# Kernel optimization log

Measured on AMD Instinct MI355X. Metric: run time of the kernel, lower is better.

Reference implementation:

```python
import jax, jax.numpy as jnp
import numpy as np

B, T, I, H = 64, 1024, 256, 512


def setup_inputs() -> dict:
    key = jax.random.key(0)
    ks = jax.random.split(key, 5)
    # Xavier-uniform-like scale: sqrt(6/(fan_in+fan_out)) ~ use small normal init
    def xavier(k, shape):
        bound = np.sqrt(6.0 / (shape[0] + shape[1])).astype(np.float32)
        return jax.random.uniform(k, shape, jnp.float32, -bound, bound)
    return {
        "x": jax.random.normal(ks[0], (B, T, I), jnp.float32),
        "W_ih0": xavier(ks[1], (I, H)),
        "W_hh0": xavier(ks[2], (H, H)),
        "b0": jnp.zeros((H,), jnp.float32),
        "W_ih1": xavier(ks[3], (H, H)),
        "W_hh1": xavier(ks[4], (H, H)),
        "b1": jnp.zeros((H,), jnp.float32),
    }


def _run_layer(xs, W_ih, W_hh, b):
    # xs: [B, T, D_in] -> ys: [B, T, H], h_last: [B, H]
    h0 = jnp.zeros((xs.shape[0], W_hh.shape[0]), xs.dtype)
    # Precompute input transform for all timesteps in one big GEMM
    x_proj = jnp.einsum('btd,dh->bth', xs, W_ih)

    def step(h, xp_t):
        h_new = jnp.tanh(xp_t + h @ W_hh + b)
        return h_new, h_new

    h_last, ys = jax.lax.scan(step, h0, jnp.swapaxes(x_proj, 0, 1))  # scan over T
    return jnp.swapaxes(ys, 0, 1), h_last


def reference(x, W_ih0, W_hh0, b0, W_ih1, W_hh1, b1):
    out0, h0n = _run_layer(x, W_ih0, W_hh0, b0)
    out1, h1n = _run_layer(out0, W_ih1, W_hh1, b1)
    h_n = jnp.stack([h0n, h1n], axis=0)  # [num_layers, B, H]
    return out1, h_n
```

## Files before the change

kernel.cpp:

```cpp
#include <hip/hip_runtime.h>
#include <cstdint>

#define B_  64
#define T_  1024
#define I_  256
#define H_  512

typedef _Float16 h2_t __attribute__((ext_vector_type(2)));
typedef int sv16 __attribute__((ext_vector_type(16)));

__device__ __forceinline__ uint16_t f2h(float f) {
  _Float16 h = (_Float16)f;
  return __builtin_bit_cast(uint16_t, h);
}
__device__ __forceinline__ float dot2(uint32_t a, uint32_t b, float c) {
  return __builtin_amdgcn_fdot2(__builtin_bit_cast(h2_t, a),
                                __builtin_bit_cast(h2_t, b), c, false);
}
__device__ __forceinline__ float fast_tanh(float s) {
  float e = __expf(2.0f * s);
  return fmaf(-2.0f, __builtin_amdgcn_rcpf(e + 1.0f), 1.0f);
}

template<int P>
__device__ __forceinline__ uint32_t hsel(sv16 h0, sv16 h1, sv16 h2, sv16 h3) {
  if constexpr (P < 16)      return (uint32_t)h0[P];
  else if constexpr (P < 32) return (uint32_t)h1[P - 16];
  else if constexpr (P < 48) return (uint32_t)h2[P - 32];
  else                       return (uint32_t)h3[P - 48];
}

__global__ void pack_whh(const float* __restrict__ W, uint32_t* __restrict__ out) {
  int idx = blockIdx.x * 256 + threadIdx.x;
  int k8 = idx >> 11;
  int j  = (idx >> 2) & 511;
  int m  = idx & 3;
  int k  = k8 * 8 + m * 2;
  uint32_t lo = f2h(W[k * H_ + j]);
  uint32_t hi = f2h(W[(k + 1) * H_ + j]);
  out[idx] = lo | (hi << 16);
}

template<int K>
__global__ __launch_bounds__(256) void gemm_rows(const float* A,
    const float* __restrict__ W, const float* __restrict__ bias,
    float* Y) {
  __shared__ float As[64 * (K + 1)];
  const int tid = threadIdx.x;
  const size_t row0 = (size_t)blockIdx.x * 64;
  const float* Ab = A + row0 * K;
  for (int idx = tid * 4; idx < 64 * K; idx += 1024) {
    float4 v = *(const float4*)(Ab + idx);
    int rr = idx / K;
    int cc = idx - rr * K;
    float* dst = &As[rr * (K + 1) + cc];
    dst[0] = v.x; dst[1] = v.y; dst[2] = v.z; dst[3] = v.w;
  }
  __syncthreads();
  const int cg = tid & 15;
  const int rg = tid >> 4;
  float acc[4][32];
  #pragma unroll
  for (int i = 0; i < 32; ++i) {
    float bz = bias[cg + 16 * i];
    acc[0][i] = bz; acc[1][i] = bz; acc[2][i] = bz; acc[3][i] = bz;
  }
  const float* Wc = W + cg;
  for (int k = 0; k < K; ++k) {
    float a0 = As[(rg * 4 + 0) * (K + 1) + k];
    float a1 = As[(rg * 4 + 1) * (K + 1) + k];
    float a2 = As[(rg * 4 + 2) * (K + 1) + k];
    float a3 = As[(rg * 4 + 3) * (K + 1) + k];
    const float* Wk = Wc + (size_t)k * H_;
    #pragma unroll
    for (int i = 0; i < 32; ++i) {
      float w = Wk[16 * i];
      acc[0][i] = fmaf(a0, w, acc[0][i]);
      acc[1][i] = fmaf(a1, w, acc[1][i]);
      acc[2][i] = fmaf(a2, w, acc[2][i]);
      acc[3][i] = fmaf(a3, w, acc[3][i]);
    }
  }
  float* Yb = Y + row0 * H_;
  #pragma unroll
  for (int jj = 0; jj < 4; ++jj) {
    float* Yr = Yb + (size_t)(rg * 4 + jj) * H_ + cg;
    #pragma unroll
    for (int i = 0; i < 32; ++i) Yr[16 * i] = acc[jj][i];
  }
}

#define ROW(m, WEXPR) { uint4 w_ = (WEXPR); \
  a0 = dot2(w_.x, hsel<4*(m)+0>(h0,h1,h2,h3), a0); \
  a1 = dot2(w_.y, hsel<4*(m)+1>(h0,h1,h2,h3), a1); \
  a2 = dot2(w_.z, hsel<4*(m)+2>(h0,h1,h2,h3), a2); \
  a3 = dot2(w_.w, hsel<4*(m)+3>(h0,h1,h2,h3), a3); }

#define BATCH_LOAD(OFF0, OFF1, OFF2, OFF3) \
  asm volatile("s_load_dwordx16 %0, %4, " OFF0 "\n\t" \
               "s_load_dwordx16 %1, %4, " OFF1 "\n\t" \
               "s_load_dwordx16 %2, %4, " OFF2 "\n\t" \
               "s_load_dwordx16 %3, %4, " OFF3 \
               : "=s"(h0), "=s"(h1), "=s"(h2), "=s"(h3) : "s"(hbase)); \
  asm volatile("s_waitcnt lgkmcnt(0)" : "+s"(h0), "+s"(h1), "+s"(h2), "+s"(h3)); \
  __builtin_amdgcn_sched_barrier(0);

#define CONS16(W0)  ROW(0,W0(0))  ROW(1,W0(1))  ROW(2,W0(2))  ROW(3,W0(3)) \
                    ROW(4,W0(4))  ROW(5,W0(5))  ROW(6,W0(6))  ROW(7,W0(7)) \
                    ROW(8,W0(8))  ROW(9,W0(9))  ROW(10,W0(10)) ROW(11,W0(11)) \
                    ROW(12,W0(12)) ROW(13,W0(13)) ROW(14,W0(14)) ROW(15,W0(15))

#define WREG0(m) wrv[m]
#define WREG1(m) wrv[16 + (m)]
#define WLDS(m)  WL[(m) * 512 + j]
#define WSTR(m)  g[m]

__global__ __launch_bounds__(512, 2) void rnn_scan(float* Y,
    const uint4* __restrict__ Wp, ushort* __restrict__ hb16,
    float* __restrict__ hn) {
  __shared__ uint4 WL[16 * 512];
  const int j = threadIdx.x;
  float* Yb = Y + (size_t)blockIdx.x * (T_ * H_);
  ushort* hbp = hb16 + blockIdx.x * H_;

  uint4 wrv[32];
  #pragma unroll
  for (int m = 0; m < 32; ++m) wrv[m] = Wp[m * H_ + j];
  #pragma unroll
  for (int it = 0; it < 16; ++it) WL[it * 512 + j] = Wp[(32 + it) * 512 + j];

  float xp0 = Yb[j];
  float v = fast_tanh(xp0);
  hbp[j] = f2h(v);
  Yb[j] = v;
  const uint64_t hbase = (uint64_t)(uintptr_t)hbp;
  asm volatile("s_waitcnt vmcnt(0) lgkmcnt(0)\n\ts_barrier\n\ts_dcache_inv" ::: "memory");

  for (int t = 1; t < T_; ++t) {
    float xpt = Yb[t * H_ + j];
    uint4 g[16];
    #pragma unroll
    for (int m = 0; m < 16; ++m) g[m] = Wp[(48 + m) * H_ + j];
    float a0 = 0.f, a1 = 0.f, a2 = 0.f, a3 = 0.f;
    sv16 h0, h1, h2, h3;
    BATCH_LOAD("0x0", "0x40", "0x80", "0xc0")
    CONS16(WREG0)
    BATCH_LOAD("0x100", "0x140", "0x180", "0x1c0")
    CONS16(WREG1)
    BATCH_LOAD("0x200", "0x240", "0x280", "0x2c0")
    CONS16(WLDS)
    BATCH_LOAD("0x300", "0x340", "0x380", "0x3c0")
    CONS16(WSTR)

    float s = xpt + ((a0 + a1) + (a2 + a3));
    v = fast_tanh(s);
    hbp[j] = f2h(v);
    Yb[t * H_ + j] = v;
    asm volatile("s_waitcnt vmcnt(0)\n\ts_barrier\n\ts_dcache_inv" ::: "memory");
  }
  hn[blockIdx.x * H_ + j] = v;
}

extern "C" void kernel_launch(void* const* d_in, const int* in_sizes, int n_in,
                              void* d_out, int out_size, void* d_ws, size_t ws_size,
                              hipStream_t stream) {
  const float* x     = (const float*)d_in[0];
  const float* W_ih0 = (const float*)d_in[1];
  const float* W_hh0 = (const float*)d_in[2];
  const float* b0    = (const float*)d_in[3];
  const float* W_ih1 = (const float*)d_in[4];
  const float* W_hh1 = (const float*)d_in[5];
  const float* b1    = (const float*)d_in[6];

  float* Y  = (float*)d_out;
  float* hn = Y + (size_t)B_ * T_ * H_;
  uint32_t* Wp = (uint32_t*)d_ws;
  ushort* hbuf = (ushort*)((char*)d_ws + 512 * 1024);

  pack_whh<<<512, 256, 0, stream>>>(W_hh0, Wp);
  gemm_rows<I_><<<1024, 256, 0, stream>>>(x, W_ih0, b0, Y);
  rnn_scan<<<B_, H_, 0, stream>>>(Y, (const uint4*)Wp, hbuf, hn);
  pack_whh<<<512, 256, 0, stream>>>(W_hh1, Wp);
  gemm_rows<H_><<<1024, 256, 0, stream>>>(Y, W_ih1, b1, Y);
  rnn_scan<<<B_, H_, 0, stream>>>(Y, (const uint4*)Wp, hbuf, hn + B_ * H_);
}
```

Measured before the change: 4.183 ms.

## Keep more W_hh in registers, drop LDS, double-buffer hidden state

The recurrent kernel now keeps 48 of the 64 packed W_hh row groups in VGPRs and drops the LDS copy. The remaining 16 groups are streamed from global memory in four-chunk pieces, each prefetched one batch ahead so the load overlaps the dot-product work. The fp16 hidden state is ping-ponged between two buffers, and the barrier is moved ahead of the Y store so that store is no longer waited on before the next step. The cost is much higher register pressure (192 VGPRs for weights under launch_bounds 512,2), which risks spills, and the hidden-state workspace doubles in size.

```diff
diff --git a/kernel.cpp b/kernel.cpp
--- a/kernel.cpp
+++ b/kernel.cpp
@@ -100,63 +100,79 @@
   asm volatile("s_load_dwordx16 %0, %4, " OFF0 "\n\t" \
                "s_load_dwordx16 %1, %4, " OFF1 "\n\t" \
                "s_load_dwordx16 %2, %4, " OFF2 "\n\t" \
-               "s_load_dwordx16 %3, %4, " OFF3 \
-               : "=s"(h0), "=s"(h1), "=s"(h2), "=s"(h3) : "s"(hbase)); \
-  asm volatile("s_waitcnt lgkmcnt(0)" : "+s"(h0), "+s"(h1), "+s"(h2), "+s"(h3)); \
+               "s_load_dwordx16 %3, %4, " OFF3 "\n\t" \
+               "s_waitcnt lgkmcnt(0)" \
+               : "=&s"(h0), "=&s"(h1), "=&s"(h2), "=&s"(h3) : "s"(hbase)); \
   __builtin_amdgcn_sched_barrier(0);
 
-#define CONS16(W0)  ROW(0,W0(0))  ROW(1,W0(1))  ROW(2,W0(2))  ROW(3,W0(3)) \
-                    ROW(4,W0(4))  ROW(5,W0(5))  ROW(6,W0(6))  ROW(7,W0(7)) \
-                    ROW(8,W0(8))  ROW(9,W0(9))  ROW(10,W0(10)) ROW(11,W0(11)) \
-                    ROW(12,W0(12)) ROW(13,W0(13)) ROW(14,W0(14)) ROW(15,W0(15))
-
-#define WREG0(m) wrv[m]
-#define WREG1(m) wrv[16 + (m)]
-#define WLDS(m)  WL[(m) * 512 + j]
-#define WSTR(m)  g[m]
+#define CONSQ(q, G) \
+  ROW(0,  wrv[12*(q)+0])  ROW(1,  wrv[12*(q)+1])  ROW(2,  wrv[12*(q)+2]) \
+  ROW(3,  wrv[12*(q)+3])  ROW(4,  wrv[12*(q)+4])  ROW(5,  wrv[12*(q)+5]) \
+  ROW(6,  wrv[12*(q)+6])  ROW(7,  wrv[12*(q)+7])  ROW(8,  wrv[12*(q)+8]) \
+  ROW(9,  wrv[12*(q)+9])  ROW(10, wrv[12*(q)+10]) ROW(11, wrv[12*(q)+11]) \
+  ROW(12, G[0]) ROW(13, G[1]) ROW(14, G[2]) ROW(15, G[3])
 
 __global__ __launch_bounds__(512, 2) void rnn_scan(float* Y,
     const uint4* __restrict__ Wp, ushort* __restrict__ hb16,
     float* __restrict__ hn) {
-  __shared__ uint4 WL[16 * 512];
   const int j = threadIdx.x;
   float* Yb = Y + (size_t)blockIdx.x * (T_ * H_);
-  ushort* hbp = hb16 + blockIdx.x * H_;
-
-  uint4 wrv[32];
-  #pragma unroll
-  for (int m = 0; m < 32; ++m) wrv[m] = Wp[m * H_ + j];
-  #pragma unroll
-  for (int it = 0; it < 16; ++it) WL[it * 512 + j] = Wp[(32 + it) * 512 + j];
+  ushort* hp0 = hb16 + blockIdx.x * (2 * H_);
+  ushort* hp1 = hp0 + H_;
+
+  uint4 wrv[48];
+  #pragma unroll
+  for (int q = 0; q < 4; ++q)
+    #pragma unroll
+    for (int r = 0; r < 12; ++r)
+      wrv[12 * q + r] = Wp[(16 * q + r) * H_ + j];
+  #pragma unroll
+  for (int m = 0; m < 48; ++m)
+    asm volatile("" : "+v"(wrv[m].x), "+v"(wrv[m].y), "+v"(wrv[m].z), "+v"(wrv[m].w));
 
   float xp0 = Yb[j];
   float v = fast_tanh(xp0);
-  hbp[j] = f2h(v);
+  hp0[j] = f2h(v);
   Yb[j] = v;
-  const uint64_t hbase = (uint64_t)(uintptr_t)hbp;
+  const uint64_t hb0 = (uint64_t)(uintptr_t)hp0;
+  const uint64_t hb1 = (uint64_t)(uintptr_t)hp1;
   asm volatile("s_waitcnt vmcnt(0) lgkmcnt(0)\n\ts_barrier\n\ts_dcache_inv" ::: "memory");
 
+  const uint4* WpS = Wp + j;
+
   for (int t = 1; t < T_; ++t) {
+    const uint64_t hbase = (t & 1) ? hb0 : hb1;
+    ushort* hst = (t & 1) ? hp1 : hp0;
     float xpt = Yb[t * H_ + j];
-    uint4 g[16];
-    #pragma unroll
-    for (int m = 0; m < 16; ++m) g[m] = Wp[(48 + m) * H_ + j];
     float a0 = 0.f, a1 = 0.f, a2 = 0.f, a3 = 0.f;
     sv16 h0, h1, h2, h3;
+    uint4 gA[4], gB[4];
+    #pragma unroll
+    for (int s = 0; s < 4; ++s) gA[s] = WpS[(12 + s) * H_];
+
     BATCH_LOAD("0x0", "0x40", "0x80", "0xc0")
-    CONS16(WREG0)
+    #pragma unroll
+    for (int s = 0; s < 4; ++s) gB[s] = WpS[(28 + s) * H_];
+    CONSQ(0, gA)
+
     BATCH_LOAD("0x100", "0x140", "0x180", "0x1c0")
-    CONS16(WREG1)
+    #pragma unroll
+    for (int s = 0; s < 4; ++s) gA[s] = WpS[(44 + s) * H_];
+    CONSQ(1, gB)
+
     BATCH_LOAD("0x200", "0x240", "0x280", "0x2c0")
-    CONS16(WLDS)
+    #pragma unroll
+    for (int s = 0; s < 4; ++s) gB[s] = WpS[(60 + s) * H_];
+    CONSQ(2, gA)
+
     BATCH_LOAD("0x300", "0x340", "0x380", "0x3c0")
-    CONS16(WSTR)
+    CONSQ(3, gB)
 
     float s = xpt + ((a0 + a1) + (a2 + a3));
     v = fast_tanh(s);
-    hbp[j] = f2h(v);
+    hst[j] = f2h(v);
+    asm volatile("s_waitcnt vmcnt(0)\n\ts_barrier\n\ts_dcache_inv" ::: "memory");
     Yb[t * H_ + j] = v;
-    asm volatile("s_waitcnt vmcnt(0)\n\ts_barrier\n\ts_dcache_inv" ::: "memory");
   }
   hn[blockIdx.x * H_ + j] = v;
 }
```

Result: slower. 10.20 ms (+144.0%).
